# Kernel optimization log

Measured on AMD Instinct MI355X. Metric: run time of the kernel, lower is better.

## Reference

```python
import math
import jax, jax.numpy as jnp
import numpy as np

N, S, D = 1024, 256, 256
C, R, CLASSES = 256, 64, 1000


def setup_inputs() -> dict:
    key = jax.random.key(0)
    ks = jax.random.split(key, 10)
    inv_sqrt_d = 1.0 / math.sqrt(D)
    return {
        "q": jax.random.normal(ks[0], (N, D), dtype=jnp.float32),
        "K": jax.random.normal(ks[1], (N, S, D), dtype=jnp.float32),
        "V": jax.random.normal(ks[2], (N, S, D), dtype=jnp.float32),
        "codebook": jax.random.normal(ks[3], (C, D), dtype=jnp.float32) * inv_sqrt_d,
        "residual_codebook": jax.random.normal(ks[4], (R, D), dtype=jnp.float32) * inv_sqrt_d,
        "Wq": jax.random.normal(ks[5], (D, D), dtype=jnp.float32) * inv_sqrt_d,
        "residual_logit": jnp.zeros((), dtype=jnp.float32),
        "Wc": jax.random.normal(ks[6], (CLASSES, D), dtype=jnp.float32) * inv_sqrt_d,
        "bc": jnp.zeros((CLASSES,), dtype=jnp.float32),
        "Wr": jax.random.normal(ks[7], (D, D), dtype=jnp.float32) * inv_sqrt_d,
        "br": jnp.zeros((D,), dtype=jnp.float32),
    }


def reference(q, K, V, codebook, residual_codebook, Wq, residual_logit, Wc, bc, Wr, br):
    scale = math.sqrt(q.shape[-1])
    q_proj = q @ Wq.T  # [N,D]

    # --- base codebook pass ---
    code_weights = jax.nn.softmax(jnp.einsum('nd,cd->nc', q_proj, codebook) / scale, axis=-1)
    slot_code_weights = jax.nn.softmax(jnp.einsum('nsd,cd->nsc', K, codebook) / scale, axis=-1)
    slot_code_summaries = jnp.einsum('nsc,nsd->ncd', slot_code_weights, V)
    base_summary = jnp.einsum('nc,ncd->nd', code_weights, slot_code_summaries)
    base_weights = jnp.einsum('nc,nsc->ns', code_weights, slot_code_weights)

    # --- residual quantization pass ---
    query_residual = q_proj - code_weights @ codebook
    slot_residual = K - jnp.einsum('nsc,cd->nsd', slot_code_weights, codebook)
    residual_code_weights = jax.nn.softmax(
        jnp.einsum('nd,rd->nr', query_residual, residual_codebook) / scale, axis=-1)
    residual_slot_code_weights = jax.nn.softmax(
        jnp.einsum('nsd,rd->nsr', slot_residual, residual_codebook) / scale, axis=-1)
    residual_slot_summaries = jnp.einsum('nsr,nsd->nrd', residual_slot_code_weights, V)
    residual_summary = jnp.einsum('nr,nrd->nd', residual_code_weights, residual_slot_summaries)
    residual_weights = jnp.einsum('nr,nsr->ns', residual_code_weights, residual_slot_code_weights)

    gate = jax.nn.sigmoid(residual_logit)
    summary = base_summary + gate * residual_summary
    effective_weights = (base_weights + gate * residual_weights) / (1.0 + gate)

    logits = summary @ Wc.T + bc
    recon = summary @ Wr.T + br
    return (logits, recon, effective_weights)
```

## Files before the change

kernel.cpp:

```cpp
#include <hip/hip_runtime.h>
#include <hip/hip_bf16.h>
#include <math.h>

#define N_   1024
#define S_   256
#define D_   256
#define C_   256
#define R_   64
#define CLS_ 1000
#define INV16 0.0625f

typedef unsigned short ushortT;
typedef unsigned int uint32;
typedef short bf8 __attribute__((ext_vector_type(8)));
typedef float f4 __attribute__((ext_vector_type(4)));

static __device__ __forceinline__ float bf2f(uint32 u){
  return __uint_as_float(u << 16);
}
static __device__ __forceinline__ ushortT f2bf(float f){
  uint32 x = __float_as_uint(f);
  uint32 r = x + 0x7FFFu + ((x >> 16) & 1u);
  return (ushortT)(r >> 16);
}
static __device__ __forceinline__ uint32 packbf(float a, float b){
  return ((uint32)f2bf(b) << 16) | (uint32)f2bf(a);
}
static __device__ __forceinline__ float wred_max(float v){
  for (int o = 32; o; o >>= 1) v = fmaxf(v, __shfl_xor(v, o));
  return v;
}
static __device__ __forceinline__ float wred_sum(float v){
  for (int o = 32; o; o >>= 1) v += __shfl_xor(v, o);
  return v;
}
static __device__ __forceinline__ int swz(int row, int colbyte){
  return row*512 + ((colbyte & ~15) ^ ((row & 7) << 4)) + (colbyte & 15);
}
static __device__ __forceinline__ int pkidx(int row, int col, int nfrag){
  int ks = col >> 5, hi = (col >> 3) & 3, e = col & 7;
  int frag = row >> 4, l15p = row & 15;
  return ((ks*nfrag + frag)*64 + hi*16 + l15p)*8 + e;
}

__global__ __launch_bounds__(256) void k0(const float* __restrict__ cb,
    const float* __restrict__ rcb, const float* __restrict__ Wc,
    const float* __restrict__ Wr, ushortT* __restrict__ a1pk,
    ushortT* __restrict__ Wcr_bf, float* __restrict__ MT_f32,
    ushortT* __restrict__ mtpk)
{
  __shared__ float rl[D_];
  int bid = blockIdx.x, t = threadIdx.x;
  int gtid = bid*256 + t;
  int stride = gridDim.x*256;
  for (int e = gtid; e < (C_ + R_)*D_; e += stride){
    int row = e >> 8, col = e & 255;
    float v = (row < C_) ? cb[e] : rcb[e - C_*D_];
    a1pk[pkidx(row, col, 20)] = f2bf(v);
  }
  for (int e = gtid; e < CLS_*D_; e += stride) Wcr_bf[e] = f2bf(Wc[e]);
  for (int e = gtid; e < D_*D_; e += stride)  Wcr_bf[CLS_*D_ + e] = f2bf(Wr[e]);
  for (int e = gtid; e < 24*D_; e += stride)  Wcr_bf[1256*D_ + e] = 0;

  if (bid < R_){
    rl[t] = rcb[bid*D_ + t];
    __syncthreads();
    float acc = 0.f;
    const float* crow = cb + t*D_;
    #pragma unroll 8
    for (int k = 0; k < D_; k += 4){
      float4 w = *(const float4*)(crow + k);
      acc += w.x*rl[k] + w.y*rl[k+1] + w.z*rl[k+2] + w.w*rl[k+3];
    }
    MT_f32[bid*C_ + t] = acc;
    mtpk[pkidx(bid, t, 4)] = f2bf(acc);
  }
}

#define G4 4
__global__ __launch_bounds__(256) void k1(const float* __restrict__ q,
    const float* __restrict__ cb, const float* __restrict__ rcb,
    const float* __restrict__ Wq, const float* __restrict__ MT_f32,
    float* __restrict__ cw_ws, float* __restrict__ rcw_ws)
{
  __shared__ float qv[G4][D_], qp[G4][D_], cwl[G4][C_];
  __shared__ float redA[G4][4], redB2[G4][4];
  int n0 = blockIdx.x*G4, t = threadIdx.x;
  #pragma unroll
  for (int g = 0; g < G4; g++) qv[g][t] = q[(n0+g)*D_ + t];
  __syncthreads();
  {
    float acc[G4] = {0.f,0.f,0.f,0.f};
    const float* wrow = Wq + t*D_;
    #pragma unroll 4
    for (int k = 0; k < D_; k += 4){
      float4 w = *(const float4*)(wrow + k);
      #pragma unroll
      for (int g = 0; g < G4; g++)
        acc[g] += qv[g][k]*w.x + qv[g][k+1]*w.y + qv[g][k+2]*w.z + qv[g][k+3]*w.w;
    }
    #pragma unroll
    for (int g = 0; g < G4; g++) qp[g][t] = acc[g];
  }
  __syncthreads();
  float L[G4] = {0.f,0.f,0.f,0.f};
  {
    const float* crow = cb + t*D_;
    #pragma unroll 4
    for (int k = 0; k < D_; k += 4){
      float4 w = *(const float4*)(crow + k);
      #pragma unroll
      for (int g = 0; g < G4; g++)
        L[g] += qp[g][k]*w.x + qp[g][k+1]*w.y + qp[g][k+2]*w.z + qp[g][k+3]*w.w;
    }
  }
  float m[G4], e[G4], s[G4];
  #pragma unroll
  for (int g = 0; g < G4; g++){ L[g] *= INV16; m[g] = wred_max(L[g]); }
  if ((t & 63) == 0)
    #pragma unroll
    for (int g = 0; g < G4; g++) redA[g][t >> 6] = m[g];
  __syncthreads();
  #pragma unroll
  for (int g = 0; g < G4; g++){
    m[g] = fmaxf(fmaxf(redA[g][0], redA[g][1]), fmaxf(redA[g][2], redA[g][3]));
    e[g] = __expf(L[g] - m[g]);
    s[g] = wred_sum(e[g]);
  }
  if ((t & 63) == 0)
    #pragma unroll
    for (int g = 0; g < G4; g++) redB2[g][t >> 6] = s[g];
  __syncthreads();
  #pragma unroll
  for (int g = 0; g < G4; g++){
    float ss = redB2[g][0] + redB2[g][1] + redB2[g][2] + redB2[g][3];
    float w = e[g] / ss;
    cwl[g][t] = w;
    cw_ws[(n0+g)*C_ + t] = w;
  }
  __syncthreads();
  if (t < R_){
    float qd[G4] = {0.f,0.f,0.f,0.f}, md[G4] = {0.f,0.f,0.f,0.f};
    const float* rrow = rcb + t*D_;
    const float* mrow = MT_f32 + t*C_;
    #pragma unroll 4
    for (int k = 0; k < D_; k += 4){
      float4 wv = *(const float4*)(rrow + k);
      float4 mv = *(const float4*)(mrow + k);
      #pragma unroll
      for (int g = 0; g < G4; g++){
        qd[g] += qp[g][k]*wv.x + qp[g][k+1]*wv.y + qp[g][k+2]*wv.z + qp[g][k+3]*wv.w;
        md[g] += cwl[g][k]*mv.x + cwl[g][k+1]*mv.y + cwl[g][k+2]*mv.z + cwl[g][k+3]*mv.w;
      }
    }
    #pragma unroll
    for (int g = 0; g < G4; g++){
      float Lr = (qd[g] - md[g]) * INV16;
      float mr = wred_max(Lr);
      float er = __expf(Lr - mr);
      float sr = wred_sum(er);
      rcw_ws[(n0+g)*R_ + t] = er / sr;
    }
  }
}

__global__ __launch_bounds__(256, 4) void k2a(const float* __restrict__ Kt,
    const ushortT* __restrict__ a1pk, const ushortT* __restrict__ mtpk,
    const float* __restrict__ cw_ws, const float* __restrict__ rcw_ws,
    const float* __restrict__ rlogit, float* __restrict__ comb_ws,
    float* __restrict__ out_ew)
{
  __shared__ __align__(16) ushortT Ktile[32*256];
  __shared__ __align__(16) ushortT Wtile[32*256];
  __shared__ float redS[4][32], redW[4][32];
  __shared__ float red3S[4][32], red3W[4][32];

  int bx  = blockIdx.x;
  int n   = bx >> 3;
  int s0  = (bx & 7) * 32;
  int tid = threadIdx.x;
  int lane = tid & 63, w = tid >> 6;
  int l15 = lane & 15, l4 = lane >> 4;
  int rp  = w >> 1;
  int sjr = w & 1;
  float gate  = 1.f / (1.f + __expf(-rlogit[0]));
  float inv1g = 1.f / (1.f + gate);

  const float* Kn = Kt + (size_t)n*S_*D_ + (size_t)s0*D_;

  #pragma unroll
  for (int j = 0; j < 4; j++){
    int ch = tid + j*256;
    int row = ch >> 5, blk = ch & 31;
    const float* src = Kn + row*D_ + blk*8;
    float4 a = *(const float4*)src;
    float4 b = *(const float4*)(src + 4);
    uint4 wv = {packbf(a.x,a.y), packbf(a.z,a.w), packbf(b.x,b.y), packbf(b.z,b.w)};
    *(uint4*)((char*)Ktile + swz(row, blk*16)) = wv;
  }
  __syncthreads();

  const ushortT* a1b = a1pk + (size_t)lane*8;
  bf8 bnxC[4], bnxR[2];
  #pragma unroll
  for (int f = 0; f < 4; f++)
    bnxC[f] = *(const bf8*)(a1b + (size_t)((w + 4*f)*64)*8);
  #pragma unroll
  for (int i = 0; i < 2; i++)
    bnxR[i] = *(const bf8*)(a1b + (size_t)((16 + 2*rp + i)*64)*8);
  f4 accC[4][2]; f4 accR[2];
  accR[0] = (f4)0.f; accR[1] = (f4)0.f;
  #pragma unroll
  for (int f = 0; f < 4; f++){ accC[f][0] = (f4)0.f; accC[f][1] = (f4)0.f; }
  #pragma unroll
  for (int ks = 0; ks < 8; ks++){
    bf8 kf0 = *(const bf8*)((const char*)Ktile + swz(     l15, ks*64 + l4*16));
    bf8 kf1 = *(const bf8*)((const char*)Ktile + swz(16 + l15, ks*64 + l4*16));
    bf8 kfr = sjr ? kf1 : kf0;
    #pragma unroll
    for (int f = 0; f < 4; f++){
      bf8 aC = bnxC[f];
      if (ks < 7)
        bnxC[f] = *(const bf8*)(a1b + (size_t)(((ks+1)*20 + w + 4*f)*64)*8);
      accC[f][0] = __builtin_amdgcn_mfma_f32_16x16x32_bf16(aC, kf0, accC[f][0], 0, 0, 0);
      accC[f][1] = __builtin_amdgcn_mfma_f32_16x16x32_bf16(aC, kf1, accC[f][1], 0, 0, 0);
    }
    #pragma unroll
    for (int i = 0; i < 2; i++){
      bf8 aR = bnxR[i];
      if (ks < 7)
        bnxR[i] = *(const bf8*)(a1b + (size_t)(((ks+1)*20 + 16 + 2*rp + i)*64)*8);
      accR[i] = __builtin_amdgcn_mfma_f32_16x16x32_bf16(aR, kfr, accR[i], 0, 0, 0);
    }
  }

  const ushortT* mtb = mtpk + (size_t)lane*8;
  bf8 mnx[2];
  #pragma unroll
  for (int i = 0; i < 2; i++)
    mnx[i] = *(const bf8*)(mtb + (size_t)((2*rp + i)*64)*8);

  float4 cwv[4];
  #pragma unroll
  for (int f = 0; f < 4; f++)
    cwv[f] = *(const float4*)(cw_ws + n*C_ + (w + 4*f)*16 + l4*4);
  float se[2] = {0,0}, sb[2] = {0,0};
  #pragma unroll
  for (int f = 0; f < 4; f++){
    int cbyte = ((w + 4*f)*16 + l4*4) * 2;
    #pragma unroll
    for (int sj = 0; sj < 2; sj++){
      float e0 = __expf(accC[f][sj][0] * INV16);
      float e1 = __expf(accC[f][sj][1] * INV16);
      float e2 = __expf(accC[f][sj][2] * INV16);
      float e3 = __expf(accC[f][sj][3] * INV16);
      se[sj] += (e0 + e1) + (e2 + e3);
      sb[sj] += e0*cwv[f].x + e1*cwv[f].y + e2*cwv[f].z + e3*cwv[f].w;
      int s_ = sj*16 + l15;
      *(uint32*)((char*)Wtile + swz(s_, cbyte))     = packbf(e0, e1);
      *(uint32*)((char*)Wtile + swz(s_, cbyte + 4)) = packbf(e2, e3);
    }
  }
  #pragma unroll
  for (int sj = 0; sj < 2; sj++){
    se[sj] += __shfl_xor(se[sj], 16); se[sj] += __shfl_xor(se[sj], 32);
    sb[sj] += __shfl_xor(sb[sj], 16); sb[sj] += __shfl_xor(sb[sj], 32);
  }
  if (l4 == 0){
    #pragma unroll
    for (int sj = 0; sj < 2; sj++){
      redS[w][sj*16 + l15] = se[sj];
      redW[w][sj*16 + l15] = sb[sj];
    }
  }
  __syncthreads();

  float bw_q, rcp_q;
  {
    int sq = sjr*16 + l15;
    float sS = redS[0][sq] + redS[1][sq] + redS[2][sq] + redS[3][sq];
    float sW = redW[0][sq] + redW[1][sq] + redW[2][sq] + redW[3][sq];
    rcp_q = 1.f / sS;
    bw_q  = sW * rcp_q;
  }

  f4 wm[2]; wm[0] = (f4)0.f; wm[1] = (f4)0.f;
  #pragma unroll
  for (int ks = 0; ks < 8; ks++){
    bf8 wb = *(const bf8*)((const char*)Wtile + swz(sjr*16 + l15, ks*64 + l4*16));
    #pragma unroll
    for (int i = 0; i < 2; i++){
      bf8 a = mnx[i];
      if (ks < 7)
        mnx[i] = *(const bf8*)(mtb + (size_t)(((ks+1)*4 + 2*rp + i)*64)*8);
      wm[i] = __builtin_amdgcn_mfma_f32_16x16x32_bf16(a, wb, wm[i], 0, 0, 0);
    }
  }

  float se3 = 0.f, sc3 = 0.f;
  #pragma unroll
  for (int i = 0; i < 2; i++){
    float4 rv = *(const float4*)(rcw_ws + n*R_ + (2*rp + i)*16 + l4*4);
    float e0 = __expf((accR[i][0] - wm[i][0]*rcp_q) * INV16);
    float e1 = __expf((accR[i][1] - wm[i][1]*rcp_q) * INV16);
    float e2 = __expf((accR[i][2] - wm[i][2]*rcp_q) * INV16);
    float e3 = __expf((accR[i][3] - wm[i][3]*rcp_q) * INV16);
    se3 += (e0 + e1) + (e2 + e3);
    sc3 += e0*rv.x + e1*rv.y + e2*rv.z + e3*rv.w;
  }
  se3 += __shfl_xor(se3, 16); se3 += __shfl_xor(se3, 32);
  sc3 += __shfl_xor(sc3, 16); sc3 += __shfl_xor(sc3, 32);
  if (l4 == 0){
    red3S[w][sjr*16 + l15] = se3;
    red3W[w][sjr*16 + l15] = sc3;
  }
  __syncthreads();

  if (w < 2){
    int sq = w*16 + l15;
    float sS3 = red3S[w][sq] + red3S[w + 2][sq];
    float sW3 = red3W[w][sq] + red3W[w + 2][sq];
    float comb = bw_q + gate * (sW3 / sS3);
    if (l4 == 0){
      int sabs = n*S_ + s0 + sq;
      out_ew[sabs]  = comb * inv1g;
      comb_ws[sabs] = comb;
    }
  }
}

__global__ __launch_bounds__(256) void k2b(const float* __restrict__ Vt,
    const float* __restrict__ comb_ws, float* __restrict__ sum_ws)
{
  __shared__ float cl[S_];
  __shared__ float4 part[4][64];
  int n = blockIdx.x, tid = threadIdx.x;
  int lane = tid & 63, w = tid >> 6;
  cl[tid] = comb_ws[n*S_ + tid];
  __syncthreads();
  const float* Vn = Vt + (size_t)n*S_*D_ + (size_t)(w*64)*D_ + lane*4;
  float4 a0 = {0,0,0,0}, a1 = {0,0,0,0};
  #pragma unroll 8
  for (int j = 0; j < 64; j += 2){
    float4 v0 = *(const float4*)(Vn + (size_t)j*D_);
    float4 v1 = *(const float4*)(Vn + (size_t)(j+1)*D_);
    float c0 = cl[w*64 + j], c1 = cl[w*64 + j + 1];
    a0.x = fmaf(c0, v0.x, a0.x); a0.y = fmaf(c0, v0.y, a0.y);
    a0.z = fmaf(c0, v0.z, a0.z); a0.w = fmaf(c0, v0.w, a0.w);
    a1.x = fmaf(c1, v1.x, a1.x); a1.y = fmaf(c1, v1.y, a1.y);
    a1.z = fmaf(c1, v1.z, a1.z); a1.w = fmaf(c1, v1.w, a1.w);
  }
  float4 acc = {a0.x+a1.x, a0.y+a1.y, a0.z+a1.z, a0.w+a1.w};
  part[w][lane] = acc;
  __syncthreads();
  if (tid < 64){
    float4 p0 = part[0][tid], p1 = part[1][tid], p2 = part[2][tid], p3 = part[3][tid];
    float4 r = {p0.x+p1.x+p2.x+p3.x, p0.y+p1.y+p2.y+p3.y,
                p0.z+p1.z+p2.z+p3.z, p0.w+p1.w+p2.w+p3.w};
    *(float4*)(sum_ws + (size_t)n*D_ + tid*4) = r;
  }
}

__global__ __launch_bounds__(256) void k3(const float* __restrict__ sum_ws,
    const ushortT* __restrict__ Wcr_bf, const float* __restrict__ bc,
    const float* __restrict__ br, float* __restrict__ out)
{
  __shared__ __align__(16) ushortT Stile[64*256];
  int bx = blockIdx.x;
  int ot = bx >> 4;
  int nt = bx & 15;
  int tid = threadIdx.x;
  int lane = tid & 63, wid = tid >> 6;
  int l15 = lane & 15, l4 = lane >> 4;

  const float* Sp = sum_ws + (size_t)nt*64*D_;
  #pragma unroll
  for (int j = 0; j < 8; j++){
    int ch = tid + j*256;
    int row = ch >> 5, blk = ch & 31;
    const float* src = Sp + row*D_ + blk*8;
    float4 a = *(const float4*)src;
    float4 b = *(const float4*)(src + 4);
    uint4 wv = {packbf(a.x,a.y), packbf(a.z,a.w), packbf(b.x,b.y), packbf(b.z,b.w)};
    *(uint4*)((char*)Stile + swz(row, blk*16)) = wv;
  }
  __syncthreads();

  int o0 = ot*64 + wid*16;
  const ushortT* Ap = Wcr_bf + (size_t)(o0 + l15)*D_ + l4*8;
  f4 acc[4];
  #pragma unroll
  for (int j = 0; j < 4; j++) acc[j] = (f4)0.f;
  #pragma unroll
  for (int k = 0; k < 8; k++){
    bf8 a = *(const bf8*)(Ap + k*32);
    #pragma unroll
    for (int nj = 0; nj < 4; nj++){
      bf8 b = *(const bf8*)((const char*)Stile + swz(nj*16 + l15, k*64 + l4*16));
      acc[nj] = __builtin_amdgcn_mfma_f32_16x16x32_bf16(a, b, acc[nj], 0, 0, 0);
    }
  }
  int obase = o0 + l4*4;
  if (obase < 1256){
    float4 bias;
    if (obase < CLS_) bias = *(const float4*)(bc + obase);
    else              bias = *(const float4*)(br + (obase - CLS_));
    #pragma unroll
    for (int nj = 0; nj < 4; nj++){
      int nn = nt*64 + nj*16 + l15;
      float4 v = {acc[nj][0]+bias.x, acc[nj][1]+bias.y, acc[nj][2]+bias.z, acc[nj][3]+bias.w};
      if (obase < CLS_) *(float4*)(out + (size_t)nn*CLS_ + obase) = v;
      else              *(float4*)(out + (size_t)N_*CLS_ + (size_t)nn*D_ + (obase - CLS_)) = v;
    }
  }
}

extern "C" void kernel_launch(void* const* d_in, const int* in_sizes, int n_in,
                              void* d_out, int out_size, void* d_ws, size_t ws_size,
                              hipStream_t stream)
{
  const float* q    = (const float*)d_in[0];
  const float* Kt   = (const float*)d_in[1];
  const float* Vt   = (const float*)d_in[2];
  const float* cb   = (const float*)d_in[3];
  const float* rcb  = (const float*)d_in[4];
  const float* Wq   = (const float*)d_in[5];
  const float* rlg  = (const float*)d_in[6];
  const float* Wc   = (const float*)d_in[7];
  const float* bc   = (const float*)d_in[8];
  const float* Wr   = (const float*)d_in[9];
  const float* br   = (const float*)d_in[10];
  float* out = (float*)d_out;
  float* ws  = (float*)d_ws;

  float* cw_ws   = ws;
  float* rcw_ws  = ws + 262144;
  float* sum_ws  = ws + 327680;
  float* comb_ws = ws + 589824;
  float* MT_f32  = ws + 851968;
  ushortT* a1pk   = (ushortT*)(ws + 868352);
  ushortT* mtpk   = a1pk + (C_ + R_)*D_;
  ushortT* Wcr_bf = mtpk + R_*C_;

  float* out_logits = out;
  float* out_ew     = out + (size_t)N_*CLS_ + (size_t)N_*D_;

  k0 <<<128,   256, 0, stream>>>(cb, rcb, Wc, Wr, a1pk, Wcr_bf, MT_f32, mtpk);
  k1 <<<N_/G4, 256, 0, stream>>>(q, cb, rcb, Wq, MT_f32, cw_ws, rcw_ws);
  k2a<<<N_*8,  256, 0, stream>>>(Kt, a1pk, mtpk, cw_ws, rcw_ws, rlg, comb_ws, out_ew);
  k2b<<<N_,    256, 0, stream>>>(Vt, comb_ws, sum_ws);
  k3 <<<320,   256, 0, stream>>>(sum_ws, Wcr_bf, bc, br, out_logits);
}
```

Measured before the change: 224.6 us.

## Make k2a persistent per row with double-buffered async K loads into LDS

k2a now runs one 512-thread block per query row instead of eight 256-thread blocks per row. The block walks the 32-slot tiles in a loop and prefetches the next fp32 K tile into a second LDS buffer with global_load_lds. K is kept as fp32 in LDS and converted to bf16 when the MFMA fragment is read, replacing the old register round-trip and pack before the LDS store. The aim is to hide K load latency behind the MFMA and softmax work and to cut per-block setup and launch overhead. The cost is roughly 80KB of LDS per block, which may limit occupancy, fewer blocks to fill the CUs, and reliance on barriers to cover the async load completion.

```diff
diff --git a/kernel.cpp b/kernel.cpp
--- a/kernel.cpp
+++ b/kernel.cpp
@@ -41,6 +41,21 @@
   int ks = col >> 5, hi = (col >> 3) & 3, e = col & 7;
   int frag = row >> 4, l15p = row & 15;
   return ((ks*nfrag + frag)*64 + hi*16 + l15p)*8 + e;
+}
+static __device__ __forceinline__ void gload_lds16(const float* src, float* dst){
+  __builtin_amdgcn_global_load_lds(
+      (const __attribute__((address_space(1))) unsigned int*)src,
+      (__attribute__((address_space(3))) unsigned int*)dst, 16, 0, 0);
+}
+static __device__ __forceinline__ bf8 kf_read(const float* buf, int row, int c0){
+  int x = row & 7;
+  const char* base = (const char*)buf + row*1024;
+  float4 fa = *(const float4*)(base + ((c0    ) ^ x)*16);
+  float4 fb = *(const float4*)(base + ((c0 + 1) ^ x)*16);
+  union { bf8 v; uint32 u[4]; } t;
+  t.u[0] = packbf(fa.x, fa.y); t.u[1] = packbf(fa.z, fa.w);
+  t.u[2] = packbf(fb.x, fb.y); t.u[3] = packbf(fb.z, fb.w);
+  return t.v;
 }
 
 __global__ __launch_bounds__(256) void k0(const float* __restrict__ cb,
@@ -164,167 +179,167 @@
   }
 }
 
-__global__ __launch_bounds__(256, 4) void k2a(const float* __restrict__ Kt,
+__global__ __launch_bounds__(512, 2) void k2a(const float* __restrict__ Kt,
     const ushortT* __restrict__ a1pk, const ushortT* __restrict__ mtpk,
     const float* __restrict__ cw_ws, const float* __restrict__ rcw_ws,
     const float* __restrict__ rlogit, float* __restrict__ comb_ws,
     float* __restrict__ out_ew)
 {
-  __shared__ __align__(16) ushortT Ktile[32*256];
+  __shared__ __align__(16) float  Kbuf[2][32*256];
   __shared__ __align__(16) ushortT Wtile[32*256];
-  __shared__ float redS[4][32], redW[4][32];
+  __shared__ float redS[8][32], redW[8][32];
   __shared__ float red3S[4][32], red3W[4][32];
 
-  int bx  = blockIdx.x;
-  int n   = bx >> 3;
-  int s0  = (bx & 7) * 32;
+  int n   = blockIdx.x;
   int tid = threadIdx.x;
   int lane = tid & 63, w = tid >> 6;
   int l15 = lane & 15, l4 = lane >> 4;
-  int rp  = w >> 1;
-  int sjr = w & 1;
+  int sjw = w >> 2;
+  int rfw = w & 3;
   float gate  = 1.f / (1.f + __expf(-rlogit[0]));
   float inv1g = 1.f / (1.f + gate);
 
-  const float* Kn = Kt + (size_t)n*S_*D_ + (size_t)s0*D_;
+  const float* Kn = Kt + (size_t)n*S_*D_;
+  const ushortT* a1b = a1pk + (size_t)lane*8;
+  const ushortT* mtb = mtpk + (size_t)lane*8;
+
+  float4 cwv[2];
+  #pragma unroll
+  for (int f = 0; f < 2; f++)
+    cwv[f] = *(const float4*)(cw_ws + n*C_ + (w + 8*f)*16 + l4*4);
+  float4 rcwv = *(const float4*)(rcw_ws + n*R_ + rfw*16 + l4*4);
 
   #pragma unroll
   for (int j = 0; j < 4; j++){
-    int ch = tid + j*256;
-    int row = ch >> 5, blk = ch & 31;
-    const float* src = Kn + row*D_ + blk*8;
-    float4 a = *(const float4*)src;
-    float4 b = *(const float4*)(src + 4);
-    uint4 wv = {packbf(a.x,a.y), packbf(a.z,a.w), packbf(b.x,b.y), packbf(b.z,b.w)};
-    *(uint4*)((char*)Ktile + swz(row, blk*16)) = wv;
-  }
-  __syncthreads();
-
-  const ushortT* a1b = a1pk + (size_t)lane*8;
-  bf8 bnxC[4], bnxR[2];
-  #pragma unroll
-  for (int f = 0; f < 4; f++)
-    bnxC[f] = *(const bf8*)(a1b + (size_t)((w + 4*f)*64)*8);
-  #pragma unroll
-  for (int i = 0; i < 2; i++)
-    bnxR[i] = *(const bf8*)(a1b + (size_t)((16 + 2*rp + i)*64)*8);
-  f4 accC[4][2]; f4 accR[2];
-  accR[0] = (f4)0.f; accR[1] = (f4)0.f;
-  #pragma unroll
-  for (int f = 0; f < 4; f++){ accC[f][0] = (f4)0.f; accC[f][1] = (f4)0.f; }
-  #pragma unroll
-  for (int ks = 0; ks < 8; ks++){
-    bf8 kf0 = *(const bf8*)((const char*)Ktile + swz(     l15, ks*64 + l4*16));
-    bf8 kf1 = *(const bf8*)((const char*)Ktile + swz(16 + l15, ks*64 + l4*16));
-    bf8 kfr = sjr ? kf1 : kf0;
-    #pragma unroll
-    for (int f = 0; f < 4; f++){
-      bf8 aC = bnxC[f];
+    int r = w*4 + j;
+    gload_lds16(Kn + (size_t)r*D_ + ((lane ^ (r & 7)) << 2), &Kbuf[0][r*256]);
+  }
+  __syncthreads();
+
+  #pragma unroll
+  for (int t = 0; t < 8; t++){
+    const float* buf = Kbuf[t & 1];
+    if (t < 7){
+      const float* KnT = Kn + (size_t)(t + 1)*32*D_;
+      float* nbuf = Kbuf[(t + 1) & 1];
+      #pragma unroll
+      for (int j = 0; j < 4; j++){
+        int r = w*4 + j;
+        gload_lds16(KnT + (size_t)r*D_ + ((lane ^ (r & 7)) << 2), &nbuf[r*256]);
+      }
+    }
+
+    bf8 bnxC[2], bnxR;
+    bnxC[0] = *(const bf8*)(a1b + (size_t)(w)*512);
+    bnxC[1] = *(const bf8*)(a1b + (size_t)(w + 8)*512);
+    bnxR    = *(const bf8*)(a1b + (size_t)(16 + rfw)*512);
+    f4 accC[2][2]; f4 accR = (f4)0.f;
+    accC[0][0] = (f4)0.f; accC[0][1] = (f4)0.f;
+    accC[1][0] = (f4)0.f; accC[1][1] = (f4)0.f;
+    #pragma unroll
+    for (int ks = 0; ks < 8; ks++){
+      bf8 kf0 = kf_read(buf,      l15, ks*8 + l4*2);
+      bf8 kf1 = kf_read(buf, 16 + l15, ks*8 + l4*2);
+      #pragma unroll
+      for (int f = 0; f < 2; f++){
+        bf8 aC = bnxC[f];
+        if (ks < 7)
+          bnxC[f] = *(const bf8*)(a1b + (size_t)((ks+1)*20 + w + 8*f)*512);
+        accC[f][0] = __builtin_amdgcn_mfma_f32_16x16x32_bf16(aC, kf0, accC[f][0], 0, 0, 0);
+        accC[f][1] = __builtin_amdgcn_mfma_f32_16x16x32_bf16(aC, kf1, accC[f][1], 0, 0, 0);
+      }
+      bf8 aR = bnxR;
       if (ks < 7)
-        bnxC[f] = *(const bf8*)(a1b + (size_t)(((ks+1)*20 + w + 4*f)*64)*8);
-      accC[f][0] = __builtin_amdgcn_mfma_f32_16x16x32_bf16(aC, kf0, accC[f][0], 0, 0, 0);
-      accC[f][1] = __builtin_amdgcn_mfma_f32_16x16x32_bf16(aC, kf1, accC[f][1], 0, 0, 0);
-    }
-    #pragma unroll
-    for (int i = 0; i < 2; i++){
-      bf8 aR = bnxR[i];
-      if (ks < 7)
-        bnxR[i] = *(const bf8*)(a1b + (size_t)(((ks+1)*20 + 16 + 2*rp + i)*64)*8);
-      accR[i] = __builtin_amdgcn_mfma_f32_16x16x32_bf16(aR, kfr, accR[i], 0, 0, 0);
-    }
-  }
-
-  const ushortT* mtb = mtpk + (size_t)lane*8;
-  bf8 mnx[2];
-  #pragma unroll
-  for (int i = 0; i < 2; i++)
-    mnx[i] = *(const bf8*)(mtb + (size_t)((2*rp + i)*64)*8);
-
-  float4 cwv[4];
-  #pragma unroll
-  for (int f = 0; f < 4; f++)
-    cwv[f] = *(const float4*)(cw_ws + n*C_ + (w + 4*f)*16 + l4*4);
-  float se[2] = {0,0}, sb[2] = {0,0};
-  #pragma unroll
-  for (int f = 0; f < 4; f++){
-    int cbyte = ((w + 4*f)*16 + l4*4) * 2;
+        bnxR = *(const bf8*)(a1b + (size_t)((ks+1)*20 + 16 + rfw)*512);
+      bf8 kfr = sjw ? kf1 : kf0;
+      accR = __builtin_amdgcn_mfma_f32_16x16x32_bf16(aR, kfr, accR, 0, 0, 0);
+    }
+
+    float se[2] = {0.f, 0.f}, sb[2] = {0.f, 0.f};
+    #pragma unroll
+    for (int f = 0; f < 2; f++){
+      int cbyte = ((w + 8*f)*16 + l4*4) * 2;
+      #pragma unroll
+      for (int sj = 0; sj < 2; sj++){
+        float e0 = __expf(accC[f][sj][0] * INV16);
+        float e1 = __expf(accC[f][sj][1] * INV16);
+        float e2 = __expf(accC[f][sj][2] * INV16);
+        float e3 = __expf(accC[f][sj][3] * INV16);
+        se[sj] += (e0 + e1) + (e2 + e3);
+        sb[sj] += e0*cwv[f].x + e1*cwv[f].y + e2*cwv[f].z + e3*cwv[f].w;
+        int s_ = sj*16 + l15;
+        *(uint32*)((char*)Wtile + swz(s_, cbyte))     = packbf(e0, e1);
+        *(uint32*)((char*)Wtile + swz(s_, cbyte + 4)) = packbf(e2, e3);
+      }
+    }
     #pragma unroll
     for (int sj = 0; sj < 2; sj++){
-      float e0 = __expf(accC[f][sj][0] * INV16);
-      float e1 = __expf(accC[f][sj][1] * INV16);
-      float e2 = __expf(accC[f][sj][2] * INV16);
-      float e3 = __expf(accC[f][sj][3] * INV16);
-      se[sj] += (e0 + e1) + (e2 + e3);
-      sb[sj] += e0*cwv[f].x + e1*cwv[f].y + e2*cwv[f].z + e3*cwv[f].w;
-      int s_ = sj*16 + l15;
-      *(uint32*)((char*)Wtile + swz(s_, cbyte))     = packbf(e0, e1);
-      *(uint32*)((char*)Wtile + swz(s_, cbyte + 4)) = packbf(e2, e3);
-    }
-  }
-  #pragma unroll
-  for (int sj = 0; sj < 2; sj++){
-    se[sj] += __shfl_xor(se[sj], 16); se[sj] += __shfl_xor(se[sj], 32);
-    sb[sj] += __shfl_xor(sb[sj], 16); sb[sj] += __shfl_xor(sb[sj], 32);
-  }
-  if (l4 == 0){
-    #pragma unroll
-    for (int sj = 0; sj < 2; sj++){
-      redS[w][sj*16 + l15] = se[sj];
-      redW[w][sj*16 + l15] = sb[sj];
-    }
-  }
-  __syncthreads();
-
-  float bw_q, rcp_q;
-  {
-    int sq = sjr*16 + l15;
-    float sS = redS[0][sq] + redS[1][sq] + redS[2][sq] + redS[3][sq];
-    float sW = redW[0][sq] + redW[1][sq] + redW[2][sq] + redW[3][sq];
-    rcp_q = 1.f / sS;
-    bw_q  = sW * rcp_q;
-  }
-
-  f4 wm[2]; wm[0] = (f4)0.f; wm[1] = (f4)0.f;
-  #pragma unroll
-  for (int ks = 0; ks < 8; ks++){
-    bf8 wb = *(const bf8*)((const char*)Wtile + swz(sjr*16 + l15, ks*64 + l4*16));
-    #pragma unroll
-    for (int i = 0; i < 2; i++){
-      bf8 a = mnx[i];
-      if (ks < 7)
-        mnx[i] = *(const bf8*)(mtb + (size_t)(((ks+1)*4 + 2*rp + i)*64)*8);
-      wm[i] = __builtin_amdgcn_mfma_f32_16x16x32_bf16(a, wb, wm[i], 0, 0, 0);
-    }
-  }
-
-  float se3 = 0.f, sc3 = 0.f;
-  #pragma unroll
-  for (int i = 0; i < 2; i++){
-    float4 rv = *(const float4*)(rcw_ws + n*R_ + (2*rp + i)*16 + l4*4);
-    float e0 = __expf((accR[i][0] - wm[i][0]*rcp_q) * INV16);
-    float e1 = __expf((accR[i][1] - wm[i][1]*rcp_q) * INV16);
-    float e2 = __expf((accR[i][2] - wm[i][2]*rcp_q) * INV16);
-    float e3 = __expf((accR[i][3] - wm[i][3]*rcp_q) * INV16);
-    se3 += (e0 + e1) + (e2 + e3);
-    sc3 += e0*rv.x + e1*rv.y + e2*rv.z + e3*rv.w;
-  }
-  se3 += __shfl_xor(se3, 16); se3 += __shfl_xor(se3, 32);
-  sc3 += __shfl_xor(sc3, 16); sc3 += __shfl_xor(sc3, 32);
-  if (l4 == 0){
-    red3S[w][sjr*16 + l15] = se3;
-    red3W[w][sjr*16 + l15] = sc3;
-  }
-  __syncthreads();
-
-  if (w < 2){
-    int sq = w*16 + l15;
-    float sS3 = red3S[w][sq] + red3S[w + 2][sq];
-    float sW3 = red3W[w][sq] + red3W[w + 2][sq];
-    float comb = bw_q + gate * (sW3 / sS3);
+      se[sj] += __shfl_xor(se[sj], 16); se[sj] += __shfl_xor(se[sj], 32);
+      sb[sj] += __shfl_xor(sb[sj], 16); sb[sj] += __shfl_xor(sb[sj], 32);
+    }
     if (l4 == 0){
-      int sabs = n*S_ + s0 + sq;
-      out_ew[sabs]  = comb * inv1g;
-      comb_ws[sabs] = comb;
+      #pragma unroll
+      for (int sj = 0; sj < 2; sj++){
+        redS[w][sj*16 + l15] = se[sj];
+        redW[w][sj*16 + l15] = sb[sj];
+      }
+    }
+    __syncthreads();
+
+    int colr = sjw*16 + l15;
+    float rcp_q;
+    {
+      float sS = 0.f;
+      #pragma unroll
+      for (int i = 0; i < 8; i++) sS += redS[i][colr];
+      rcp_q = 1.f / sS;
+    }
+    float bwc = 0.f;
+    if (w < 2){
+      int colb = w*16 + l15;
+      float sS = 0.f, sW = 0.f;
+      #pragma unroll
+      for (int i = 0; i < 8; i++){ sS += redS[i][colb]; sW += redW[i][colb]; }
+      bwc = sW / sS;
+    }
+
+    bf8 mnx = *(const bf8*)(mtb + (size_t)(rfw)*512);
+    f4 wm = (f4)0.f;
+    #pragma unroll
+    for (int ks = 0; ks < 8; ks++){
+      bf8 wb = *(const bf8*)((const char*)Wtile + swz(sjw*16 + l15, ks*64 + l4*16));
+      bf8 a = mnx;
+      if (ks < 7) mnx = *(const bf8*)(mtb + (size_t)((ks+1)*4 + rfw)*512);
+      wm = __builtin_amdgcn_mfma_f32_16x16x32_bf16(a, wb, wm, 0, 0, 0);
+    }
+
+    float se3, sc3;
+    {
+      float e0 = __expf((accR[0] - wm[0]*rcp_q) * INV16);
+      float e1 = __expf((accR[1] - wm[1]*rcp_q) * INV16);
+      float e2 = __expf((accR[2] - wm[2]*rcp_q) * INV16);
+      float e3 = __expf((accR[3] - wm[3]*rcp_q) * INV16);
+      se3 = (e0 + e1) + (e2 + e3);
+      sc3 = e0*rcwv.x + e1*rcwv.y + e2*rcwv.z + e3*rcwv.w;
+    }
+    se3 += __shfl_xor(se3, 16); se3 += __shfl_xor(se3, 32);
+    sc3 += __shfl_xor(sc3, 16); sc3 += __shfl_xor(sc3, 32);
+    if (l4 == 0){
+      red3S[rfw][colr] = se3;
+      red3W[rfw][colr] = sc3;
+    }
+    __syncthreads();
+
+    if (w < 2){
+      int col = w*16 + l15;
+      float sS3 = red3S[0][col] + red3S[1][col] + red3S[2][col] + red3S[3][col];
+      float sW3 = red3W[0][col] + red3W[1][col] + red3W[2][col] + red3W[3][col];
+      float comb = bwc + gate * (sW3 / sS3);
+      if (l4 == 0){
+        int sabs = n*S_ + t*32 + col;
+        out_ew[sabs]  = comb * inv1g;
+        comb_ws[sabs] = comb;
+      }
     }
   }
 }
@@ -447,7 +462,7 @@
 
   k0 <<<128,   256, 0, stream>>>(cb, rcb, Wc, Wr, a1pk, Wcr_bf, MT_f32, mtpk);
   k1 <<<N_/G4, 256, 0, stream>>>(q, cb, rcb, Wq, MT_f32, cw_ws, rcw_ws);
-  k2a<<<N_*8,  256, 0, stream>>>(Kt, a1pk, mtpk, cw_ws, rcw_ws, rlg, comb_ws, out_ew);
+  k2a<<<N_,    512, 0, stream>>>(Kt, a1pk, mtpk, cw_ws, rcw_ws, rlg, comb_ws, out_ew);
   k2b<<<N_,    256, 0, stream>>>(Vt, comb_ws, sum_ws);
   k3 <<<320,   256, 0, stream>>>(sum_ws, Wcr_bf, bc, br, out_logits);
 }
```

New measurement: 284.0 us. 26.5% more time.

## Fuse V-weighted summary into k2a with atomic accumulation, drop k2b

Applied to the files above, without the earlier changes.

Folds the V-weighted summation into the end of the K-scoring kernel. Each block now multiplies its 32 slots' combined weights against V and atomically adds the partial sums into sum_ws, which k0 zeroes beforehand. This removes the separate k2b launch and the comb_ws round trip through global memory. In exchange it adds per-element atomics (8 blocks contend per row), more register pressure in k2a, and a summation order that is no longer deterministic.

```diff
diff --git a/kernel.cpp b/kernel.cpp
--- a/kernel.cpp
+++ b/kernel.cpp
@@ -47,7 +47,7 @@
     const float* __restrict__ rcb, const float* __restrict__ Wc,
     const float* __restrict__ Wr, ushortT* __restrict__ a1pk,
     ushortT* __restrict__ Wcr_bf, float* __restrict__ MT_f32,
-    ushortT* __restrict__ mtpk)
+    ushortT* __restrict__ mtpk, float* __restrict__ sum_ws)
 {
   __shared__ float rl[D_];
   int bid = blockIdx.x, t = threadIdx.x;
@@ -61,6 +61,7 @@
   for (int e = gtid; e < CLS_*D_; e += stride) Wcr_bf[e] = f2bf(Wc[e]);
   for (int e = gtid; e < D_*D_; e += stride)  Wcr_bf[CLS_*D_ + e] = f2bf(Wr[e]);
   for (int e = gtid; e < 24*D_; e += stride)  Wcr_bf[1256*D_ + e] = 0;
+  for (int e = gtid; e < N_*D_; e += stride)  sum_ws[e] = 0.f;
 
   if (bid < R_){
     rl[t] = rcb[bid*D_ + t];
@@ -165,15 +166,16 @@
 }
 
 __global__ __launch_bounds__(256, 4) void k2a(const float* __restrict__ Kt,
-    const ushortT* __restrict__ a1pk, const ushortT* __restrict__ mtpk,
-    const float* __restrict__ cw_ws, const float* __restrict__ rcw_ws,
-    const float* __restrict__ rlogit, float* __restrict__ comb_ws,
-    float* __restrict__ out_ew)
+    const float* __restrict__ Vt, const ushortT* __restrict__ a1pk,
+    const ushortT* __restrict__ mtpk, const float* __restrict__ cw_ws,
+    const float* __restrict__ rcw_ws, const float* __restrict__ rlogit,
+    float* __restrict__ sum_ws, float* __restrict__ out_ew)
 {
   __shared__ __align__(16) ushortT Ktile[32*256];
   __shared__ __align__(16) ushortT Wtile[32*256];
   __shared__ float redS[4][32], redW[4][32];
   __shared__ float red3S[4][32], red3W[4][32];
+  __shared__ float combl[32];
 
   int bx  = blockIdx.x;
   int n   = bx >> 3;
@@ -323,41 +325,27 @@
     float comb = bw_q + gate * (sW3 / sS3);
     if (l4 == 0){
       int sabs = n*S_ + s0 + sq;
-      out_ew[sabs]  = comb * inv1g;
-      comb_ws[sabs] = comb;
-    }
-  }
-}
-
-__global__ __launch_bounds__(256) void k2b(const float* __restrict__ Vt,
-    const float* __restrict__ comb_ws, float* __restrict__ sum_ws)
-{
-  __shared__ float cl[S_];
-  __shared__ float4 part[4][64];
-  int n = blockIdx.x, tid = threadIdx.x;
-  int lane = tid & 63, w = tid >> 6;
-  cl[tid] = comb_ws[n*S_ + tid];
-  __syncthreads();
-  const float* Vn = Vt + (size_t)n*S_*D_ + (size_t)(w*64)*D_ + lane*4;
-  float4 a0 = {0,0,0,0}, a1 = {0,0,0,0};
-  #pragma unroll 8
-  for (int j = 0; j < 64; j += 2){
-    float4 v0 = *(const float4*)(Vn + (size_t)j*D_);
-    float4 v1 = *(const float4*)(Vn + (size_t)(j+1)*D_);
-    float c0 = cl[w*64 + j], c1 = cl[w*64 + j + 1];
-    a0.x = fmaf(c0, v0.x, a0.x); a0.y = fmaf(c0, v0.y, a0.y);
-    a0.z = fmaf(c0, v0.z, a0.z); a0.w = fmaf(c0, v0.w, a0.w);
-    a1.x = fmaf(c1, v1.x, a1.x); a1.y = fmaf(c1, v1.y, a1.y);
-    a1.z = fmaf(c1, v1.z, a1.z); a1.w = fmaf(c1, v1.w, a1.w);
-  }
-  float4 acc = {a0.x+a1.x, a0.y+a1.y, a0.z+a1.z, a0.w+a1.w};
-  part[w][lane] = acc;
-  __syncthreads();
-  if (tid < 64){
-    float4 p0 = part[0][tid], p1 = part[1][tid], p2 = part[2][tid], p3 = part[3][tid];
-    float4 r = {p0.x+p1.x+p2.x+p3.x, p0.y+p1.y+p2.y+p3.y,
-                p0.z+p1.z+p2.z+p3.z, p0.w+p1.w+p2.w+p3.w};
-    *(float4*)(sum_ws + (size_t)n*D_ + tid*4) = r;
+      out_ew[sabs] = comb * inv1g;
+      combl[sq]    = comb;
+    }
+  }
+  __syncthreads();
+
+  {
+    const float* vp = Vt + (size_t)n*S_*D_ + (size_t)(s0 + w*8)*D_ + lane*4;
+    float4 sacc = {0.f, 0.f, 0.f, 0.f};
+    #pragma unroll
+    for (int j = 0; j < 8; j++){
+      float c = combl[w*8 + j];
+      float4 v = *(const float4*)(vp + (size_t)j*D_);
+      sacc.x = fmaf(c, v.x, sacc.x); sacc.y = fmaf(c, v.y, sacc.y);
+      sacc.z = fmaf(c, v.z, sacc.z); sacc.w = fmaf(c, v.w, sacc.w);
+    }
+    float* dst = sum_ws + (size_t)n*D_ + lane*4;
+    atomicAdd(dst + 0, sacc.x);
+    atomicAdd(dst + 1, sacc.y);
+    atomicAdd(dst + 2, sacc.z);
+    atomicAdd(dst + 3, sacc.w);
   }
 }
 
@@ -436,7 +424,6 @@
   float* cw_ws   = ws;
   float* rcw_ws  = ws + 262144;
   float* sum_ws  = ws + 327680;
-  float* comb_ws = ws + 589824;
   float* MT_f32  = ws + 851968;
   ushortT* a1pk   = (ushortT*)(ws + 868352);
   ushortT* mtpk   = a1pk + (C_ + R_)*D_;
@@ -445,9 +432,8 @@
   float* out_logits = out;
   float* out_ew     = out + (size_t)N_*CLS_ + (size_t)N_*D_;
 
-  k0 <<<128,   256, 0, stream>>>(cb, rcb, Wc, Wr, a1pk, Wcr_bf, MT_f32, mtpk);
+  k0 <<<128,   256, 0, stream>>>(cb, rcb, Wc, Wr, a1pk, Wcr_bf, MT_f32, mtpk, sum_ws);
   k1 <<<N_/G4, 256, 0, stream>>>(q, cb, rcb, Wq, MT_f32, cw_ws, rcw_ws);
-  k2a<<<N_*8,  256, 0, stream>>>(Kt, a1pk, mtpk, cw_ws, rcw_ws, rlg, comb_ws, out_ew);
-  k2b<<<N_,    256, 0, stream>>>(Vt, comb_ws, sum_ws);
+  k2a<<<N_*8,  256, 0, stream>>>(Kt, Vt, a1pk, mtpk, cw_ws, rcw_ws, rlg, sum_ws, out_ew);
   k3 <<<320,   256, 0, stream>>>(sum_ws, Wcr_bf, bc, br, out_logits);
 }
```

Result: slower. 247.8 us (+10.4%).
